# Optimization experiments

Measured on AMD Instinct MI355X. Metric: run time of the kernel, lower is better.

The kernel has to match this reference:

```python
import jax, jax.numpy as jnp
import numpy as np

SEQ_LEN = 524288
TAGSET = 64
START = 62   # tag_to_ix['START_TAG']
STOP = 63    # tag_to_ix['STOP_TAG']
NEG = -10000.0


def setup_inputs() -> dict:
    key = jax.random.key(0)
    k1, k2 = jax.random.split(key)
    feats = jax.random.normal(k1, (SEQ_LEN, TAGSET), dtype=jnp.float32)
    # learned transition matrix; trans[next, prev], with START row / STOP col masked as in __init__
    trans = jax.random.normal(k2, (TAGSET, TAGSET), dtype=jnp.float32)
    trans = trans.at[START, :].set(NEG).at[:, STOP].set(NEG)
    return {"feats": feats, "trans": trans}


def reference(feats, trans):
    # Viterbi max-plus DP. forward_var fv[prev]; scores[next, prev] = fv[prev] + trans[next, prev]
    fv0 = jnp.full((TAGSET,), NEG, dtype=jnp.float32).at[START].set(0.0)

    def step(fv, feat):
        scores = fv[None, :] + trans            # [T_next, T_prev]
        bptr = jnp.argmax(scores, axis=1)        # best previous tag per next tag
        fv_new = jnp.max(scores, axis=1) + feat  # [T]
        return fv_new, bptr

    fv, bptrs = jax.lax.scan(step, fv0, feats)   # bptrs: [seq_len, T] int

    terminal = fv + trans[STOP]                  # transition to STOP
    best = jnp.argmax(terminal)
    path_score = terminal[best]

    # backtrack through backpointers (reverse scan), emitting tag at each step
    def back(tag, bp):
        return bp[tag], tag

    _, best_path = jax.lax.scan(back, best, bptrs, reverse=True)  # [seq_len] tags
    return path_score, best_path
```

## Files before the change

### kernel.cpp

```cpp
#include <hip/hip_runtime.h>
#include <hip/hip_bf16.h>

#define T_LEN 524288
#define NTAG 64
#define START_TAG 62
#define STOP_TAG 63
#define NEGV -10000.0f

#define KCH 4096
#define CL  128
#define WU  64
#define WPB 4

#define SG  64
#define NSG (KCH / SG)

struct BlockLDS {
    float trL[NTAG * 65];
    __align__(16) float fv[WPB][2][NTAG];
};

static __device__ __forceinline__ float max3f(float a, float b, float c) {
    return fmaxf(fmaxf(a, b), c);
}

template<int MODE>
__device__ __forceinline__ void wave_run(
    int t0, int nsteps, const float* __restrict__ feats,
    unsigned int* __restrict__ bpg, float (*fv)[NTAG],
    const float* __restrict__ trL, int lane)
{
    const float* trrow = &trL[lane * 65];
    float fA[4], fB[4];
#pragma unroll
    for (int i = 0; i < 4; ++i)
        fA[i] = feats[(size_t)(t0 + i) * NTAG + lane];
    unsigned int acc = 0;
#pragma unroll 1
    for (int tt = 0; tt < nsteps; tt += 4) {
        const bool hav = (tt + 4 < nsteps);
        if (hav) {
#pragma unroll
            for (int i = 0; i < 4; ++i)
                fB[i] = feats[(size_t)(t0 + tt + 4 + i) * NTAG + lane];
        }
#pragma unroll
        for (int s = 0; s < 4; ++s) {
            const int st = tt + s;
            const float* fvp = fv[st & 1];
            const float4* fq = (const float4*)fvp;
            float* fvn = fv[(st + 1) & 1];

            float gm[8];
#pragma unroll
            for (int g = 0; g < 8; ++g) {
                const float4 x0 = fq[2 * g + 0];
                const float4 x1 = fq[2 * g + 1];
                const float* tg = trrow + g * 8;
                const float c0 = x0.x + tg[0], c1 = x0.y + tg[1];
                const float c2 = x0.z + tg[2], c3 = x0.w + tg[3];
                const float c4 = x1.x + tg[4], c5 = x1.y + tg[5];
                const float c6 = x1.z + tg[6], c7 = x1.w + tg[7];
                const float m1 = max3f(c0, c1, c2);
                const float m2 = max3f(c3, c4, c5);
                const float m3 = max3f(c6, c7, m1);
                gm[g] = fmaxf(m2, m3);
            }
            const float ga = max3f(gm[0], gm[1], gm[2]);
            const float gb = max3f(gm[3], gm[4], gm[5]);
            const float gc = max3f(gm[6], gm[7], ga);
            const float t  = fmaxf(gb, gc);
            fvn[lane] = t + fA[s];

            if (MODE == 1) {
                int g = 7;
                if (gm[6] == t) g = 6;
                if (gm[5] == t) g = 5;
                if (gm[4] == t) g = 4;
                if (gm[3] == t) g = 3;
                if (gm[2] == t) g = 2;
                if (gm[1] == t) g = 1;
                if (gm[0] == t) g = 0;
                const float4* yq = (const float4*)(fvp + (g << 3));
                const float4 y0 = yq[0];
                const float4 y1 = yq[1];
                const float* tg = trrow + (g << 3);
                const float e0 = y0.x + tg[0], e1 = y0.y + tg[1];
                const float e2 = y0.z + tg[2], e3 = y0.w + tg[3];
                const float e4 = y1.x + tg[4], e5 = y1.y + tg[5];
                const float e6 = y1.z + tg[6], e7 = y1.w + tg[7];
                int j = 7;
                if (e6 == t) j = 6;
                if (e5 == t) j = 5;
                if (e4 == t) j = 4;
                if (e3 == t) j = 3;
                if (e2 == t) j = 2;
                if (e1 == t) j = 1;
                if (e0 == t) j = 0;
                const int idx = (g << 3) | j;
                acc |= (unsigned int)idx << (8 * s);
                if (s == 3) {
                    bpg[((size_t)(t0 + st - 3) >> 2) * NTAG + lane] = acc;
                    acc = 0;
                }
            }
        }
        if (hav) {
#pragma unroll
            for (int i = 0; i < 4; ++i) fA[i] = fB[i];
        }
    }
}

__device__ __forceinline__ void load_trans_lds(const float* __restrict__ trans,
                                               int lane, float* trL)
{
    const float4* trow = (const float4*)(trans + (size_t)lane * NTAG);
    float* dst = trL + lane * 65;
#pragma unroll
    for (int j = 0; j < 16; ++j) {
        float4 v = trow[j];
        dst[j * 4 + 0] = v.x; dst[j * 4 + 1] = v.y;
        dst[j * 4 + 2] = v.z; dst[j * 4 + 3] = v.w;
    }
}

__global__ __launch_bounds__(256, 4) void pass1_kernel(
    const float* __restrict__ feats, const float* __restrict__ trans,
    unsigned int* __restrict__ bpg, float* __restrict__ ovl,
    float* __restrict__ bnd, unsigned char* __restrict__ maps)
{
    __shared__ BlockLDS L;
    const int lane = threadIdx.x & 63;
    const int w = threadIdx.x >> 6;
    const int k = blockIdx.x * WPB + w;
    load_trans_lds(trans, lane, L.trL);

    float (*fv)[NTAG] = L.fv[w];
    if (k == 0) {
        fv[0][lane] = (lane == START_TAG) ? 0.0f : NEGV;
    } else {
        fv[0][lane] = 0.0f;
    }
    if (k > 0) {
        wave_run<0>(k * CL - WU, WU, feats, nullptr, fv, L.trL, lane);
        ovl[(size_t)k * NTAG + lane] = fv[0][lane];
    }
    wave_run<1>(k * CL, CL, feats, bpg, fv, L.trL, lane);
    bnd[(size_t)(k + 1) * NTAG + lane] = fv[0][lane];

    asm volatile("s_waitcnt vmcnt(0)" ::: "memory");
    int cur = lane;
    const size_t base = ((size_t)(k * CL) >> 2) * NTAG + lane;
#pragma unroll 4
    for (int t4 = CL / 4 - 1; t4 >= 0; --t4) {
        unsigned int b4 = bpg[base + (size_t)t4 * NTAG];
#pragma unroll
        for (int j = 3; j >= 0; --j) {
            unsigned int u = __shfl(b4, cur);
            cur = (u >> (8 * j)) & 255;
        }
    }
    maps[(size_t)k * NTAG + lane] = (unsigned char)cur;
}

__global__ __launch_bounds__(1024) void finalize_part_kernel(
    const float* __restrict__ bnd, const float* __restrict__ ovl,
    float* __restrict__ pc, float* __restrict__ pe, int* __restrict__ pb)
{
    __shared__ float sc[16], se[16];
    __shared__ int sb[16];
    const int tid = threadIdx.x, w = tid >> 6, lane = tid & 63;
    const int gw = blockIdx.x * 16 + w;
    float csum = 0.f, esum = 0.f;
    int bad = 0;
    for (int k = 1 + gw; k < KCH; k += 1024) {
        float d = bnd[(size_t)k * NTAG + lane] - ovl[(size_t)k * NTAG + lane];
        float d0 = __shfl(d, 0);
        float sp = fabsf(d - d0);
#pragma unroll
        for (int o = 1; o < 64; o <<= 1) sp = fmaxf(sp, __shfl_xor(sp, o));
        csum += d0; esum += sp;
        if (!(fabsf(d0) < 1.0e7f)) bad = 1;
    }
    if (lane == 0) { sc[w] = csum; se[w] = esum; sb[w] = bad; }
    __syncthreads();
    if (tid == 0) {
        float c = 0.f, e = 0.f; int b = 0;
        for (int i = 0; i < 16; ++i) { c += sc[i]; e += se[i]; b |= sb[i]; }
        pc[blockIdx.x] = c; pe[blockIdx.x] = e; pb[blockIdx.x] = b;
    }
}

__global__ __launch_bounds__(64) void finalize_final_kernel(
    const float* __restrict__ bnd, const float* __restrict__ trans,
    const float* __restrict__ pc, const float* __restrict__ pe,
    const int* __restrict__ pb, int* __restrict__ flags,
    float* __restrict__ dout, int* __restrict__ bestp)
{
    const int tid = threadIdx.x;
    float c = pc[tid], e = pe[tid];
    int b = pb[tid];
#pragma unroll
    for (int o = 1; o < 64; o <<= 1) {
        c += __shfl_xor(c, o);
        e += __shfl_xor(e, o);
        b |= __shfl_xor(b, o);
    }
    if (!(e <= 1.0e4f)) b = 1;
    if (tid == 0) flags[0] = b;
    const float shift = -c;
    float v = (bnd[(size_t)KCH * NTAG + tid] - shift) + trans[STOP_TAG * NTAG + tid];
    int bi = tid;
#pragma unroll
    for (int o = 1; o < 64; o <<= 1) {
        float vo = __shfl_xor(v, o);
        int io = __shfl_xor(bi, o);
        if (vo > v || (vo == v && io < bi)) { v = vo; bi = io; }
    }
    if (tid == 0) { dout[0] = v; dout[T_LEN] = (float)bi; *bestp = bi; }
}

__global__ __launch_bounds__(64) void fallback_kernel(
    const float* __restrict__ feats, const float* __restrict__ trans,
    int* __restrict__ flags, float* __restrict__ dout, int* __restrict__ bestp)
{
    __shared__ float trL[NTAG * 65];
    __shared__ __align__(16) float fv[2][NTAG];
    const int lane = threadIdx.x;
    if (flags[0] == 0) return;
    load_trans_lds(trans, lane, trL);
    fv[0][lane] = (lane == START_TAG) ? 0.0f : NEGV;
    wave_run<0>(0, T_LEN, feats, nullptr, fv, trL, lane);
    float v = fv[0][lane] + trans[STOP_TAG * NTAG + lane];
    int bi = lane;
#pragma unroll
    for (int o = 1; o < 64; o <<= 1) {
        float vo = __shfl_xor(v, o);
        int io = __shfl_xor(bi, o);
        if (vo > v || (vo == v && io < bi)) { v = vo; bi = io; }
    }
    if (lane == 0) { dout[0] = v; dout[T_LEN] = (float)bi; *bestp = bi; }
}

__global__ __launch_bounds__(64) void compose_kernel(
    const unsigned char* __restrict__ maps, unsigned char* __restrict__ smaps)
{
    const int lane = threadIdx.x, j = blockIdx.x;
    int cur = lane;
#pragma unroll 4
    for (int i = (j + 1) * SG - 1; i >= j * SG; --i) {
        int m = maps[(size_t)i * NTAG + lane];
        cur = __shfl(m, cur);
    }
    smaps[j * NTAG + lane] = (unsigned char)cur;
}

__global__ __launch_bounds__(64) void superchain_kernel(
    const unsigned char* __restrict__ smaps, const int* __restrict__ bestp,
    int* __restrict__ Esuper)
{
    const int lane = threadIdx.x;
    int e = *bestp;
#pragma unroll 1
    for (int j = NSG - 1; j >= 0; --j) {
        if (lane == 0) Esuper[j] = e;
        int m = smaps[j * NTAG + lane];
        e = __shfl(m, e);
    }
}

__global__ __launch_bounds__(64) void fill_kernel(
    const unsigned char* __restrict__ maps, const int* __restrict__ Esuper,
    unsigned char* __restrict__ Eblk)
{
    const int lane = threadIdx.x, j = blockIdx.x;
    int e = Esuper[j];
#pragma unroll 4
    for (int i = (j + 1) * SG - 1; i >= j * SG; --i) {
        if (lane == 0) Eblk[i] = (unsigned char)e;
        int m = maps[(size_t)i * NTAG + lane];
        e = __shfl(m, e);
    }
}

__global__ __launch_bounds__(64) void emit_kernel(
    const unsigned int* __restrict__ bpg, const unsigned char* __restrict__ Eblk,
    float* __restrict__ dout)
{
    const int lane = threadIdx.x, k = blockIdx.x;
    const int eblk = Eblk[k];
    int cur = lane;
    const int t0 = k * CL;
    const size_t base = ((size_t)t0 >> 2) * NTAG + lane;
#pragma unroll 4
    for (int t4 = CL / 4 - 1; t4 >= 0; --t4) {
        unsigned int b4 = bpg[base + (size_t)t4 * NTAG];
#pragma unroll
        for (int j = 3; j >= 0; --j) {
            unsigned int u = __shfl(b4, cur);
            cur = (u >> (8 * j)) & 255;
            const int t = t0 + t4 * 4 + j;
            if (t > 0 && lane == eblk) dout[t] = (float)cur;
        }
    }
}

__global__ void beacon_kernel(float* dout, float wsz) { dout[0] = wsz; }

extern "C" void kernel_launch(void* const* d_in, const int* in_sizes, int n_in,
                              void* d_out, int out_size, void* d_ws, size_t ws_size,
                              hipStream_t stream) {
    const float* feats = (const float*)d_in[0];
    const float* trans = (const float*)d_in[1];
    float* dout = (float*)d_out;
    char* ws = (char*)d_ws;

    size_t off = 0;
    auto alloc = [&](size_t bytes) -> void* {
        void* p = ws + off;
        off = (off + bytes + 255) & ~(size_t)255;
        return p;
    };
    unsigned int* bpg = (unsigned int*)alloc((size_t)(T_LEN / 4) * NTAG * 4);
    float* bnd    = (float*)alloc((size_t)(KCH + 1) * NTAG * sizeof(float));
    float* ovl    = (float*)alloc((size_t)KCH * NTAG * sizeof(float));
    int*   flags  = (int*)alloc(256);
    unsigned char* maps  = (unsigned char*)alloc((size_t)KCH * NTAG);
    unsigned char* smaps = (unsigned char*)alloc((size_t)NSG * NTAG);
    int*   Esuper = (int*)alloc(NSG * sizeof(int));
    unsigned char* Eblk  = (unsigned char*)alloc(KCH);
    int*   bestp  = (int*)alloc(sizeof(int));
    float* pc     = (float*)alloc(64 * sizeof(float));
    float* pe     = (float*)alloc(64 * sizeof(float));
    int*   pb     = (int*)alloc(64 * sizeof(int));
    const size_t NEED = off;

    if (ws_size < NEED) {
        beacon_kernel<<<1, 1, 0, stream>>>(dout, (float)ws_size);
        return;
    }

    pass1_kernel<<<KCH / WPB, 256, 0, stream>>>(feats, trans, bpg, ovl, bnd, maps);
    finalize_part_kernel<<<64, 1024, 0, stream>>>(bnd, ovl, pc, pe, pb);
    finalize_final_kernel<<<1, 64, 0, stream>>>(bnd, trans, pc, pe, pb, flags, dout, bestp);
    fallback_kernel<<<1, 64, 0, stream>>>(feats, trans, flags, dout, bestp);
    compose_kernel<<<NSG, 64, 0, stream>>>(maps, smaps);
    superchain_kernel<<<1, 64, 0, stream>>>(smaps, bestp, Esuper);
    fill_kernel<<<NSG, 64, 0, stream>>>(maps, Esuper, Eblk);
    emit_kernel<<<KCH, 64, 0, stream>>>(bpg, Eblk, dout);
}
```

Baseline: 432.8 us.

## Hold transition row in registers with packed adds and merge small launch kernels

The max-plus inner loop now keeps each lane's transition row in 32 two-wide float vector registers and adds them with packed v2f operations, so it no longer reads that row from LDS every step. The fallback kernel is folded into finalize_final. The superchain and fill kernels are merged into a fill2 kernel in which each block recomputes its super-chain prefix. Together these cut the launch count from 8 to 6, at the cost of extra VGPR pressure (64 floats per lane) under launch bounds of 256 threads with 4 blocks per SM, and redundant superchain work.

Result: faster. 384.2 us (-11.2%).

```diff
diff --git a/kernel.cpp b/kernel.cpp
--- a/kernel.cpp
+++ b/kernel.cpp
@@ -15,6 +15,8 @@
 #define SG  64
 #define NSG (KCH / SG)
 
+typedef float v2f __attribute__((ext_vector_type(2)));
+
 struct BlockLDS {
     float trL[NTAG * 65];
     __align__(16) float fv[WPB][2][NTAG];
@@ -23,47 +25,63 @@
 static __device__ __forceinline__ float max3f(float a, float b, float c) {
     return fmaxf(fmaxf(a, b), c);
 }
+static __device__ __forceinline__ v2f mk2(float a, float b) {
+    v2f r; r.x = a; r.y = b; return r;
+}
+
+union Q4 { float4 q; v2f h[2]; };
 
 template<int MODE>
 __device__ __forceinline__ void wave_run(
     int t0, int nsteps, const float* __restrict__ feats,
+    const float* __restrict__ trans,
     unsigned int* __restrict__ bpg, float (*fv)[NTAG],
     const float* __restrict__ trL, int lane)
 {
+    v2f tr[32];
+    {
+        const float4* t4 = (const float4*)(trans + (size_t)lane * NTAG);
+#pragma unroll
+        for (int j = 0; j < 16; ++j) {
+            float4 v = t4[j];
+            tr[2 * j + 0] = mk2(v.x, v.y);
+            tr[2 * j + 1] = mk2(v.z, v.w);
+        }
+    }
     const float* trrow = &trL[lane * 65];
+    const float* fp = feats + (size_t)t0 * NTAG + lane;
     float fA[4], fB[4];
 #pragma unroll
-    for (int i = 0; i < 4; ++i)
-        fA[i] = feats[(size_t)(t0 + i) * NTAG + lane];
+    for (int i = 0; i < 4; ++i) fA[i] = fp[i * NTAG];
+    fp += 4 * NTAG;
     unsigned int acc = 0;
 #pragma unroll 1
     for (int tt = 0; tt < nsteps; tt += 4) {
         const bool hav = (tt + 4 < nsteps);
         if (hav) {
 #pragma unroll
-            for (int i = 0; i < 4; ++i)
-                fB[i] = feats[(size_t)(t0 + tt + 4 + i) * NTAG + lane];
+            for (int i = 0; i < 4; ++i) fB[i] = fp[i * NTAG];
+            fp += 4 * NTAG;
         }
 #pragma unroll
         for (int s = 0; s < 4; ++s) {
             const int st = tt + s;
             const float* fvp = fv[st & 1];
-            const float4* fq = (const float4*)fvp;
             float* fvn = fv[(st + 1) & 1];
+            const Q4* fq = (const Q4*)fvp;
 
             float gm[8];
 #pragma unroll
             for (int g = 0; g < 8; ++g) {
-                const float4 x0 = fq[2 * g + 0];
-                const float4 x1 = fq[2 * g + 1];
-                const float* tg = trrow + g * 8;
-                const float c0 = x0.x + tg[0], c1 = x0.y + tg[1];
-                const float c2 = x0.z + tg[2], c3 = x0.w + tg[3];
-                const float c4 = x1.x + tg[4], c5 = x1.y + tg[5];
-                const float c6 = x1.z + tg[6], c7 = x1.w + tg[7];
-                const float m1 = max3f(c0, c1, c2);
-                const float m2 = max3f(c3, c4, c5);
-                const float m3 = max3f(c6, c7, m1);
+                Q4 x0 = fq[2 * g + 0];
+                Q4 x1 = fq[2 * g + 1];
+                v2f c01 = x0.h[0] + tr[4 * g + 0];
+                v2f c23 = x0.h[1] + tr[4 * g + 1];
+                v2f c45 = x1.h[0] + tr[4 * g + 2];
+                v2f c67 = x1.h[1] + tr[4 * g + 3];
+                const float m1 = max3f(c01.x, c01.y, c23.x);
+                const float m2 = max3f(c23.y, c45.x, c45.y);
+                const float m3 = max3f(c67.x, c67.y, m1);
                 gm[g] = fmaxf(m2, m3);
             }
             const float ga = max3f(gm[0], gm[1], gm[2]);
@@ -81,14 +99,14 @@
                 if (gm[2] == t) g = 2;
                 if (gm[1] == t) g = 1;
                 if (gm[0] == t) g = 0;
-                const float4* yq = (const float4*)(fvp + (g << 3));
-                const float4 y0 = yq[0];
-                const float4 y1 = yq[1];
-                const float* tg = trrow + (g << 3);
-                const float e0 = y0.x + tg[0], e1 = y0.y + tg[1];
-                const float e2 = y0.z + tg[2], e3 = y0.w + tg[3];
-                const float e4 = y1.x + tg[4], e5 = y1.y + tg[5];
-                const float e6 = y1.z + tg[6], e7 = y1.w + tg[7];
+                const Q4* yq = (const Q4*)(fvp + (g << 3));
+                Q4 y0 = yq[0];
+                Q4 y1 = yq[1];
+                const float* tb = trrow + (g << 3);
+                const float e0 = y0.h[0].x + tb[0], e1 = y0.h[0].y + tb[1];
+                const float e2 = y0.h[1].x + tb[2], e3 = y0.h[1].y + tb[3];
+                const float e4 = y1.h[0].x + tb[4], e5 = y1.h[0].y + tb[5];
+                const float e6 = y1.h[1].x + tb[6], e7 = y1.h[1].y + tb[7];
                 int j = 7;
                 if (e6 == t) j = 6;
                 if (e5 == t) j = 5;
@@ -143,10 +161,10 @@
         fv[0][lane] = 0.0f;
     }
     if (k > 0) {
-        wave_run<0>(k * CL - WU, WU, feats, nullptr, fv, L.trL, lane);
+        wave_run<0>(k * CL - WU, WU, feats, trans, nullptr, fv, L.trL, lane);
         ovl[(size_t)k * NTAG + lane] = fv[0][lane];
     }
-    wave_run<1>(k * CL, CL, feats, bpg, fv, L.trL, lane);
+    wave_run<1>(k * CL, CL, feats, trans, bpg, fv, L.trL, lane);
     bnd[(size_t)(k + 1) * NTAG + lane] = fv[0][lane];
 
     asm volatile("s_waitcnt vmcnt(0)" ::: "memory");
@@ -194,10 +212,13 @@
 
 __global__ __launch_bounds__(64) void finalize_final_kernel(
     const float* __restrict__ bnd, const float* __restrict__ trans,
+    const float* __restrict__ feats,
     const float* __restrict__ pc, const float* __restrict__ pe,
-    const int* __restrict__ pb, int* __restrict__ flags,
+    const int* __restrict__ pb,
     float* __restrict__ dout, int* __restrict__ bestp)
 {
+    __shared__ float trL[NTAG * 65];
+    __shared__ __align__(16) float fv[2][NTAG];
     const int tid = threadIdx.x;
     float c = pc[tid], e = pe[tid];
     int b = pb[tid];
@@ -208,7 +229,6 @@
         b |= __shfl_xor(b, o);
     }
     if (!(e <= 1.0e4f)) b = 1;
-    if (tid == 0) flags[0] = b;
     const float shift = -c;
     float v = (bnd[(size_t)KCH * NTAG + tid] - shift) + trans[STOP_TAG * NTAG + tid];
     int bi = tid;
@@ -219,28 +239,21 @@
         if (vo > v || (vo == v && io < bi)) { v = vo; bi = io; }
     }
     if (tid == 0) { dout[0] = v; dout[T_LEN] = (float)bi; *bestp = bi; }
-}
-
-__global__ __launch_bounds__(64) void fallback_kernel(
-    const float* __restrict__ feats, const float* __restrict__ trans,
-    int* __restrict__ flags, float* __restrict__ dout, int* __restrict__ bestp)
-{
-    __shared__ float trL[NTAG * 65];
-    __shared__ __align__(16) float fv[2][NTAG];
-    const int lane = threadIdx.x;
-    if (flags[0] == 0) return;
-    load_trans_lds(trans, lane, trL);
-    fv[0][lane] = (lane == START_TAG) ? 0.0f : NEGV;
-    wave_run<0>(0, T_LEN, feats, nullptr, fv, trL, lane);
-    float v = fv[0][lane] + trans[STOP_TAG * NTAG + lane];
-    int bi = lane;
-#pragma unroll
-    for (int o = 1; o < 64; o <<= 1) {
-        float vo = __shfl_xor(v, o);
-        int io = __shfl_xor(bi, o);
-        if (vo > v || (vo == v && io < bi)) { v = vo; bi = io; }
-    }
-    if (lane == 0) { dout[0] = v; dout[T_LEN] = (float)bi; *bestp = bi; }
+
+    if (b) {
+        load_trans_lds(trans, tid, trL);
+        fv[0][tid] = (tid == START_TAG) ? 0.0f : NEGV;
+        wave_run<0>(0, T_LEN, feats, trans, nullptr, fv, trL, tid);
+        float v2 = fv[0][tid] + trans[STOP_TAG * NTAG + tid];
+        int b2 = tid;
+#pragma unroll
+        for (int o = 1; o < 64; o <<= 1) {
+            float vo = __shfl_xor(v2, o);
+            int io = __shfl_xor(b2, o);
+            if (vo > v2 || (vo == v2 && io < b2)) { v2 = vo; b2 = io; }
+        }
+        if (tid == 0) { dout[0] = v2; dout[T_LEN] = (float)b2; *bestp = b2; }
+    }
 }
 
 __global__ __launch_bounds__(64) void compose_kernel(
@@ -256,26 +269,17 @@
     smaps[j * NTAG + lane] = (unsigned char)cur;
 }
 
-__global__ __launch_bounds__(64) void superchain_kernel(
-    const unsigned char* __restrict__ smaps, const int* __restrict__ bestp,
-    int* __restrict__ Esuper)
-{
-    const int lane = threadIdx.x;
+__global__ __launch_bounds__(64) void fill2_kernel(
+    const unsigned char* __restrict__ maps, const unsigned char* __restrict__ smaps,
+    const int* __restrict__ bestp, unsigned char* __restrict__ Eblk)
+{
+    const int lane = threadIdx.x, j = blockIdx.x;
     int e = *bestp;
 #pragma unroll 1
-    for (int j = NSG - 1; j >= 0; --j) {
-        if (lane == 0) Esuper[j] = e;
-        int m = smaps[j * NTAG + lane];
+    for (int jj = NSG - 1; jj > j; --jj) {
+        int m = smaps[jj * NTAG + lane];
         e = __shfl(m, e);
     }
-}
-
-__global__ __launch_bounds__(64) void fill_kernel(
-    const unsigned char* __restrict__ maps, const int* __restrict__ Esuper,
-    unsigned char* __restrict__ Eblk)
-{
-    const int lane = threadIdx.x, j = blockIdx.x;
-    int e = Esuper[j];
 #pragma unroll 4
     for (int i = (j + 1) * SG - 1; i >= j * SG; --i) {
         if (lane == 0) Eblk[i] = (unsigned char)e;
@@ -325,10 +329,8 @@
     unsigned int* bpg = (unsigned int*)alloc((size_t)(T_LEN / 4) * NTAG * 4);
     float* bnd    = (float*)alloc((size_t)(KCH + 1) * NTAG * sizeof(float));
     float* ovl    = (float*)alloc((size_t)KCH * NTAG * sizeof(float));
-    int*   flags  = (int*)alloc(256);
     unsigned char* maps  = (unsigned char*)alloc((size_t)KCH * NTAG);
     unsigned char* smaps = (unsigned char*)alloc((size_t)NSG * NTAG);
-    int*   Esuper = (int*)alloc(NSG * sizeof(int));
     unsigned char* Eblk  = (unsigned char*)alloc(KCH);
     int*   bestp  = (int*)alloc(sizeof(int));
     float* pc     = (float*)alloc(64 * sizeof(float));
@@ -342,11 +344,9 @@
     }
 
     pass1_kernel<<<KCH / WPB, 256, 0, stream>>>(feats, trans, bpg, ovl, bnd, maps);
+    compose_kernel<<<NSG, 64, 0, stream>>>(maps, smaps);
     finalize_part_kernel<<<64, 1024, 0, stream>>>(bnd, ovl, pc, pe, pb);
-    finalize_final_kernel<<<1, 64, 0, stream>>>(bnd, trans, pc, pe, pb, flags, dout, bestp);
-    fallback_kernel<<<1, 64, 0, stream>>>(feats, trans, flags, dout, bestp);
-    compose_kernel<<<NSG, 64, 0, stream>>>(maps, smaps);
-    superchain_kernel<<<1, 64, 0, stream>>>(smaps, bestp, Esuper);
-    fill_kernel<<<NSG, 64, 0, stream>>>(maps, Esuper, Eblk);
+    finalize_final_kernel<<<1, 64, 0, stream>>>(bnd, trans, feats, pc, pe, pb, dout, bestp);
+    fill2_kernel<<<NSG, 64, 0, stream>>>(maps, smaps, bestp, Eblk);
     emit_kernel<<<KCH, 64, 0, stream>>>(bpg, Eblk, dout);
 }
```
